# Kernel optimization log

Measured on AMD Instinct MI355X. Metric: run time of the kernel, lower is better.

The kernel has to match this reference:

```python
import jax, jax.numpy as jnp
from jax import lax
import numpy as np

B, CIN, COUT, S = 2, 64, 128, 12
H1, H2 = CIN * 4, COUT * 4          # MBConv hidden dims (expand_ratio=4)
HEADS = 8
MLP_HID = COUT * 4                   # transformer mlp_ratio=4
EPS = 1e-5


def conv1x1(x, w, b=None):
    # 1x1x1 Conv3d == channel matmul. w: [out, in], x: [B,C,H,W,D]
    y = jnp.einsum('oc,bchwd->bohwd', w, x)
    if b is not None:
        y = y + b[None, :, None, None, None]
    return y


def inorm(x, g, b):
    # InstanceNorm3d(affine=True): per-sample, per-channel over spatial dims
    m = x.mean(axis=(2, 3, 4), keepdims=True)
    v = x.var(axis=(2, 3, 4), keepdims=True)
    return (x - m) * jax.lax.rsqrt(v + EPS) * g[None, :, None, None, None] + b[None, :, None, None, None]


def gnorm(x, g, b, groups):
    Bb, C, H, W, D = x.shape
    xr = x.reshape(Bb, groups, C // groups, H, W, D)
    m = xr.mean(axis=(2, 3, 4, 5), keepdims=True)
    v = xr.var(axis=(2, 3, 4, 5), keepdims=True)
    xr = (xr - m) * jax.lax.rsqrt(v + EPS)
    return xr.reshape(Bb, C, H, W, D) * g[None, :, None, None, None] + b[None, :, None, None, None]


def dwconv3(x, w):
    # depthwise 3x3x3, stride 1, pad 1. w: [C,1,3,3,3]
    return lax.conv_general_dilated(
        x, w, window_strides=(1, 1, 1), padding=[(1, 1)] * 3,
        dimension_numbers=('NCDHW', 'OIDHW', 'NCDHW'),
        feature_group_count=x.shape[1])


def mbconv(x, ew, g1, b1, dw, g2, b2, sw1, sb1, sw2, sb2, pw, g3, b3, use_residual):
    res = x
    h = jax.nn.silu(inorm(conv1x1(x, ew), g1, b1))        # expand 1x1
    h = jax.nn.silu(inorm(dwconv3(h, dw), g2, b2))        # depthwise 3x3x3
    s = h.mean(axis=(2, 3, 4), keepdims=True)             # SE: squeeze
    s = jax.nn.silu(conv1x1(s, sw1, sb1))
    s = jax.nn.sigmoid(conv1x1(s, sw2, sb2))
    h = h * s
    h = inorm(conv1x1(h, pw), g3, b3)                     # project
    return res + h if use_residual else h


def mhsa(x, qkv_w, proj_w, proj_b):
    Bb, C, H, W, D = x.shape
    N = H * W * D
    hd = C // HEADS
    qkv = conv1x1(x, qkv_w).reshape(Bb, 3, HEADS, hd, N)
    qkv = jnp.transpose(qkv, (1, 0, 2, 4, 3))             # [3,B,h,N,hd]
    q, k, v = qkv[0], qkv[1], qkv[2]
    attn = jax.nn.softmax(jnp.einsum('bhnd,bhmd->bhnm', q, k) * (hd ** -0.5), axis=-1)
    out = jnp.einsum('bhnm,bhmd->bhnd', attn, v)          # [B,h,N,hd]
    out = jnp.transpose(out, (0, 1, 3, 2)).reshape(Bb, C, H, W, D)
    return conv1x1(out, proj_w, proj_b)


def transformer_block(x, n1g, n1b, qkv, pw, pb, n2g, n2b, mw1, mb1, mw2, mb2):
    x = x + mhsa(gnorm(x, n1g, n1b, min(32, x.shape[1])), qkv, pw, pb)
    h = gnorm(x, n2g, n2b, min(32, x.shape[1]))
    h = conv1x1(jax.nn.gelu(conv1x1(h, mw1, mb1), approximate=False), mw2, mb2)
    return x + h


def shuffle_attn(x, cw1, cw2, gng, gnb, sw):
    b, c, h, w, d = x.shape
    G = 4
    gc = c // (2 * G)  # group_channels
    x6 = x.reshape(b, G, 2 * gc, h, w, d)
    x0 = x6[:, :, :gc].reshape(b * G, gc, h, w, d)
    x1 = x6[:, :, gc:].reshape(b * G, gc, h, w, d)
    # channel branch
    a = x0.mean(axis=(2, 3, 4), keepdims=True)
    a = conv1x1(jax.nn.silu(conv1x1(a, cw1)), cw2)
    x0 = jax.nn.sigmoid(a) * x0
    # spatial branch: GroupNorm(max(1,gc//8)=2 groups) + 1x1 conv
    sgn = gnorm(x1, gng, gnb, max(1, gc // 8))
    x1 = jax.nn.sigmoid(conv1x1(sgn, sw)) * x1
    out = jnp.concatenate([x0.reshape(b, G * gc, h, w, d), x1.reshape(b, G * gc, h, w, d)], axis=1)
    # channel shuffle
    out = out.reshape(b, G, 2 * gc, h, w, d).transpose(0, 2, 1, 3, 4, 5).reshape(b, c, h, w, d)
    return out


def setup_inputs() -> dict:
    key = jax.random.key(0)
    ks = iter(jax.random.split(key, 64))
    w = lambda *shape: jax.random.normal(next(ks), shape, jnp.float32) * 0.05
    p = {}
    p['x'] = jax.random.normal(next(ks), (B, CIN, S, S, S), jnp.float32)
    # mbconv1 (in=64 -> hidden=256 -> out=128), SE reduced = 256//4 = 64
    r1 = H1 // 4
    p['m1_ew'] = w(H1, CIN); p['m1_g1'] = jnp.ones(H1); p['m1_b1'] = jnp.zeros(H1)
    p['m1_dw'] = w(H1, 1, 3, 3, 3); p['m1_g2'] = jnp.ones(H1); p['m1_b2'] = jnp.zeros(H1)
    p['m1_sw1'] = w(r1, H1); p['m1_sb1'] = jnp.zeros(r1)
    p['m1_sw2'] = w(H1, r1); p['m1_sb2'] = jnp.zeros(H1)
    p['m1_pw'] = w(COUT, H1); p['m1_g3'] = jnp.ones(COUT); p['m1_b3'] = jnp.zeros(COUT)
    # mbconv2 (in=128 -> hidden=512 -> out=128, residual), SE reduced = 512//4 = 128
    r2 = H2 // 4
    p['m2_ew'] = w(H2, COUT); p['m2_g1'] = jnp.ones(H2); p['m2_b1'] = jnp.zeros(H2)
    p['m2_dw'] = w(H2, 1, 3, 3, 3); p['m2_g2'] = jnp.ones(H2); p['m2_b2'] = jnp.zeros(H2)
    p['m2_sw1'] = w(r2, H2); p['m2_sb1'] = jnp.zeros(r2)
    p['m2_sw2'] = w(H2, r2); p['m2_sb2'] = jnp.zeros(H2)
    p['m2_pw'] = w(COUT, H2); p['m2_g3'] = jnp.ones(COUT); p['m2_b3'] = jnp.zeros(COUT)
    # transformer
    p['t_n1g'] = jnp.ones(COUT); p['t_n1b'] = jnp.zeros(COUT)
    p['t_qkv'] = w(3 * COUT, COUT)
    p['t_pw'] = w(COUT, COUT); p['t_pb'] = jnp.zeros(COUT)
    p['t_n2g'] = jnp.ones(COUT); p['t_n2b'] = jnp.zeros(COUT)
    p['t_mw1'] = w(MLP_HID, COUT); p['t_mb1'] = jnp.zeros(MLP_HID)
    p['t_mw2'] = w(COUT, MLP_HID); p['t_mb2'] = jnp.zeros(COUT)
    # shuffle attention: group_channels = 128 // 8 = 16, channel_fc reduces to 4
    gc = COUT // 8
    p['s_cw1'] = w(max(1, gc // 4), gc); p['s_cw2'] = w(gc, max(1, gc // 4))
    p['s_gng'] = jnp.ones(gc); p['s_gnb'] = jnp.zeros(gc)
    p['s_sw'] = w(gc, gc)
    return p


def reference(x, m1_ew, m1_g1, m1_b1, m1_dw, m1_g2, m1_b2, m1_sw1, m1_sb1, m1_sw2, m1_sb2, m1_pw, m1_g3, m1_b3, m2_ew, m2_g1, m2_b1, m2_dw, m2_g2, m2_b2, m2_sw1, m2_sb1, m2_sw2, m2_sb2, m2_pw, m2_g3, m2_b3, t_n1g, t_n1b, t_qkv, t_pw, t_pb, t_n2g, t_n2b, t_mw1, t_mb1, t_mw2, t_mb2, s_cw1, s_cw2, s_gng, s_gnb, s_sw):
    x = mbconv(x, m1_ew, m1_g1, m1_b1, m1_dw, m1_g2, m1_b2, m1_sw1, m1_sb1, m1_sw2, m1_sb2, m1_pw, m1_g3, m1_b3, use_residual=False)
    x = mbconv(x, m2_ew, m2_g1, m2_b1, m2_dw, m2_g2, m2_b2, m2_sw1, m2_sb1, m2_sw2, m2_sb2, m2_pw, m2_g3, m2_b3, use_residual=True)
    x = transformer_block(x, t_n1g, t_n1b, t_qkv, t_pw, t_pb, t_n2g, t_n2b, t_mw1, t_mb1, t_mw2, t_mb2)
    x = shuffle_attn(x, s_cw1, s_cw2, s_gng, s_gnb, s_sw)
    return x
```

## Files before the change

kernel.cpp:

```cpp
#include <hip/hip_runtime.h>
#include <cmath>

#define NSP 1728
#define BB  2
#define SS  12

typedef __attribute__((ext_vector_type(8))) short short8;
typedef __attribute__((ext_vector_type(4))) short short4v;
typedef __attribute__((ext_vector_type(4))) float floatx4;

__device__ __forceinline__ short f2bf(float f) {
    unsigned u = __float_as_uint(f);
    u += 0x7fff + ((u >> 16) & 1);
    return (short)(u >> 16);
}
__device__ __forceinline__ unsigned pack2bf(float a, float b) {
    unsigned ua = __float_as_uint(a); ua += 0x7fff + ((ua >> 16) & 1);
    unsigned ub = __float_as_uint(b); ub += 0x7fff + ((ub >> 16) & 1);
    return (ua >> 16) | (ub & 0xffff0000u);
}
__device__ __forceinline__ short8 ld8(const short* p) {
    short4v a = *(const short4v*)p;
    short4v b = *(const short4v*)(p + 4);
    return __builtin_shufflevector(a, b, 0, 1, 2, 3, 4, 5, 6, 7);
}
__device__ __forceinline__ float fexp2(float x) {
    float r;
    asm("v_exp_f32 %0, %1" : "=v"(r) : "v"(x));
    return r;
}

__device__ __forceinline__ void block_reduce2(float& s, float& s2) {
    __shared__ float red[8][2];
    __syncthreads();
    #pragma unroll
    for (int o = 32; o; o >>= 1) {
        s  += __shfl_down(s,  o, 64);
        s2 += __shfl_down(s2, o, 64);
    }
    int lane = threadIdx.x & 63, w = threadIdx.x >> 6;
    if (lane == 0) { red[w][0] = s; red[w][1] = s2; }
    __syncthreads();
    int nw = (blockDim.x + 63) >> 6;
    if (threadIdx.x == 0) {
        float a = 0.f, b = 0.f;
        for (int i = 0; i < nw; i++) { a += red[i][0]; b += red[i][1]; }
        red[0][0] = a; red[0][1] = b;
    }
    __syncthreads();
    s = red[0][0]; s2 = red[0][1];
}

#define WTOT 376832
__global__ __launch_bounds__(256) void prep_kernel(
        const float* __restrict__ s0, const float* __restrict__ s1,
        const float* __restrict__ s2, const float* __restrict__ s3,
        const float* __restrict__ s4, const float* __restrict__ s5,
        const float* __restrict__ s6, const float* __restrict__ s7,
        short* __restrict__ dst, float* __restrict__ stz) {
    if (blockIdx.x < 6) stz[blockIdx.x * 256 + threadIdx.x] = 0.f;
    const int offs[9] = {0, 16384, 49152, 114688, 180224, 229376, 245760, 311296, WTOT};
    const float* srcs[8] = {s0, s1, s2, s3, s4, s5, s6, s7};
    int e = blockIdx.x * 1024 + threadIdx.x * 4;
    #pragma unroll
    for (int k = 0; k < 4; k++) {
        int idx = e + k;
        if (idx >= WTOT) return;
        int seg = 0;
        while (idx >= offs[seg + 1]) seg++;
        dst[idx] = f2bf(srcs[seg][idx - offs[seg]]);
    }
}

template<int CIN, int COUT>
__global__ __launch_bounds__(256) void convm_kernel(
        const float* __restrict__ in, const short* __restrict__ wb,
        const float* __restrict__ biasc,
        const float* __restrict__ se_s,
        const float* __restrict__ sw1, const float* __restrict__ sb1,
        const float* __restrict__ sw2, const float* __restrict__ sb2, int seR,
        const float* __restrict__ fstats, const float* __restrict__ fg,
        const float* __restrict__ fb, int fgs,
        const float* __restrict__ po, const float* __restrict__ pl,
        float* __restrict__ xout,
        const float* resid, float* out, float* stats_out, int act) {
    constexpr int XP = CIN + 8;
    __shared__ float sc[CIN];
    __shared__ float sh[CIN];
    __shared__ float hid[128];
    __shared__ __align__(16) short xa[16 * XP];
    int flat = blockIdx.x;
    int b = flat / 108, mt = flat % 108;
    int n0 = mt * 16;
    int tid = threadIdx.x;

    if (po) {
        if (tid < 128) {
            int hh = tid >> 4, j = tid & 15;
            float l = 0.f;
            #pragma unroll
            for (int js = 0; js < 6; js++)
                l += pl[(size_t)((b * 8 + hh) * 6 + js) * NSP + n0 + j];
            hid[tid] = 1.f / l;
        }
        __syncthreads();
        #pragma unroll
        for (int i = 0; i < CIN / 64; i++) {
            int e = tid + i * 256;
            int ci = e >> 2;
            int jj = (e & 3) * 4;
            int hh = ci >> 4, d = ci & 15;
            float4 acc = {0.f, 0.f, 0.f, 0.f};
            #pragma unroll
            for (int js = 0; js < 6; js++) {
                float4 pv = *(const float4*)(po +
                    ((size_t)((b * 8 + hh) * 6 + js) * 16 + d) * NSP + n0 + jj);
                acc.x += pv.x; acc.y += pv.y; acc.z += pv.z; acc.w += pv.w;
            }
            float4 li = *(const float4*)(hid + hh * 16 + jj);
            xa[(jj + 0) * XP + ci] = f2bf(acc.x * li.x);
            xa[(jj + 1) * XP + ci] = f2bf(acc.y * li.y);
            xa[(jj + 2) * XP + ci] = f2bf(acc.z * li.z);
            xa[(jj + 3) * XP + ci] = f2bf(acc.w * li.w);
        }
        __syncthreads();
    } else {
    if (sw1) {
        for (int c = tid; c < CIN; c += 256) { sc[c] = se_s[b * CIN + c]; sh[c] = 0.f; }
        __syncthreads();
        for (int r = tid; r < seR; r += 256) {
            const float* wr = sw1 + (size_t)r * CIN;
            float h0 = sb1[r], h1 = 0.f, h2 = 0.f, h3 = 0.f;
            for (int c = 0; c < CIN; c += 4) {
                h0 = fmaf(wr[c],     sc[c],     h0);
                h1 = fmaf(wr[c + 1], sc[c + 1], h1);
                h2 = fmaf(wr[c + 2], sc[c + 2], h2);
                h3 = fmaf(wr[c + 3], sc[c + 3], h3);
            }
            float hv = (h0 + h1) + (h2 + h3);
            hid[r] = hv / (1.f + __expf(-hv));
        }
        __syncthreads();
        for (int ci = tid; ci < CIN; ci += 256) {
            const float* wr = sw2 + (size_t)ci * seR;
            float g0 = sb2[ci], g1 = 0.f, g2 = 0.f, g3 = 0.f;
            for (int r = 0; r < seR; r += 4) {
                g0 = fmaf(wr[r],     hid[r],     g0);
                g1 = fmaf(wr[r + 1], hid[r + 1], g1);
                g2 = fmaf(wr[r + 2], hid[r + 2], g2);
                g3 = fmaf(wr[r + 3], hid[r + 3], g3);
            }
            float gv = (g0 + g1) + (g2 + g3);
            sc[ci] = 1.f / (1.f + __expf(-gv));
        }
    } else if (fstats) {
        for (int c = tid; c < CIN; c += 256) {
            int g0 = c / fgs;
            float S = 0.f, S2 = 0.f;
            for (int k = 0; k < fgs; k++) {
                S  += fstats[(b * CIN + g0 * fgs + k) * 2];
                S2 += fstats[(b * CIN + g0 * fgs + k) * 2 + 1];
            }
            float N = fgs * (float)NSP;
            float mean = S / N, var = S2 / N - mean * mean;
            float s = rsqrtf(var + 1e-5f) * fg[c];
            sc[c] = s;
            sh[c] = fb[c] - mean * s;
        }
    } else {
        for (int c = tid; c < CIN; c += 256) { sc[c] = 1.f; sh[c] = 0.f; }
    }
    __syncthreads();

    bool dosw = (xout != nullptr) && (blockIdx.y == 0);
    #pragma unroll
    for (int i = 0; i < CIN / 64; i++) {
        int e = tid + i * 256;
        int ci = e >> 2;
        int jj = (e & 3) * 4;
        size_t gi = ((size_t)b * CIN + ci) * NSP + n0 + jj;
        float4 v4 = *(const float4*)(in + gi);
        float s_ = sc[ci], h_ = sh[ci];
        float v0 = fmaf(v4.x, s_, h_), v1 = fmaf(v4.y, s_, h_);
        float v2 = fmaf(v4.z, s_, h_), v3 = fmaf(v4.w, s_, h_);
        if (dosw) {
            float4 o; o.x = v0; o.y = v1; o.z = v2; o.w = v3;
            *(float4*)(xout + gi) = o;
        }
        xa[(jj + 0) * XP + ci] = f2bf(v0);
        xa[(jj + 1) * XP + ci] = f2bf(v1);
        xa[(jj + 2) * XP + ci] = f2bf(v2);
        xa[(jj + 3) * XP + ci] = f2bf(v3);
    }
    __syncthreads();
    }

    int lane = tid & 63, wv = tid >> 6;
    int col = lane & 15, quad = lane >> 4;
    short8 afr[CIN / 32];
    #pragma unroll
    for (int kc = 0; kc < CIN / 32; kc++)
        afr[kc] = ld8(xa + col * XP + kc * 32 + quad * 8);

    int cobase = blockIdx.y * 64 + wv * 16;
    int co = cobase + col;
    const short* wrow = wb + (size_t)co * CIN;
    floatx4 acc = {0.f, 0.f, 0.f, 0.f};
    #pragma unroll
    for (int kc = 0; kc < CIN / 32; kc++) {
        short8 bw = ld8(wrow + kc * 32 + quad * 8);
        acc = __builtin_amdgcn_mfma_f32_16x16x32_bf16(afr[kc], bw, acc, 0, 0, 0);
    }
    float bv = biasc ? biasc[co] : 0.f;
    float r0 = acc[0] + bv, r1 = acc[1] + bv, r2 = acc[2] + bv, r3 = acc[3] + bv;
    if (act == 2) {
        r0 = 0.5f * r0 * (1.f + erff(r0 * 0.70710678118654752f));
        r1 = 0.5f * r1 * (1.f + erff(r1 * 0.70710678118654752f));
        r2 = 0.5f * r2 * (1.f + erff(r2 * 0.70710678118654752f));
        r3 = 0.5f * r3 * (1.f + erff(r3 * 0.70710678118654752f));
    }
    size_t oi = ((size_t)b * COUT + co) * NSP + n0 + quad * 4;
    if (resid) {
        float4 rv = *(const float4*)(resid + oi);
        r0 += rv.x; r1 += rv.y; r2 += rv.z; r3 += rv.w;
    }
    float4 ov; ov.x = r0; ov.y = r1; ov.z = r2; ov.w = r3;
    *(float4*)(out + oi) = ov;
    if (stats_out) {
        float s  = (r0 + r1) + (r2 + r3);
        float s2 = (r0 * r0 + r1 * r1) + (r2 * r2 + r3 * r3);
        s  += __shfl_xor(s,  16, 64);
        s  += __shfl_xor(s,  32, 64);
        s2 += __shfl_xor(s2, 16, 64);
        s2 += __shfl_xor(s2, 32, 64);
        if (lane < 16) {
            atomicAdd(&stats_out[(b * COUT + cobase + lane) * 2],     s);
            atomicAdd(&stats_out[(b * COUT + cobase + lane) * 2 + 1], s2);
        }
    }
}

__global__ __launch_bounds__(256) void post_kernel(
        const float* __restrict__ p0,
        const float* __restrict__ ng, const float* __restrict__ nb,
        const float* resid, float* out, float* __restrict__ stats_out, int C) {
    int bc = blockIdx.x;
    int c  = bc % C;
    const float* a = p0 + (size_t)bc * NSP;
    float r[7];
    float s = 0.f, s2 = 0.f;
    #pragma unroll
    for (int i = 0; i < 7; i++) {
        int n = threadIdx.x + i * 256;
        if (n < NSP) { r[i] = a[n]; s += r[i]; s2 += r[i] * r[i]; }
        else r[i] = 0.f;
    }
    block_reduce2(s, s2);
    float mean = s / NSP;
    float var = s2 / NSP - mean * mean;
    float rstd = rsqrtf(var + 1e-5f);
    float gc = ng[c], bc2 = nb[c];
    float os = 0.f, os2 = 0.f;
    #pragma unroll
    for (int i = 0; i < 7; i++) {
        int n = threadIdx.x + i * 256;
        if (n < NSP) {
            float v = (r[i] - mean) * rstd * gc + bc2;
            size_t oi = (size_t)bc * NSP + n;
            if (resid) v += resid[oi];
            out[oi] = v;
            os += v; os2 += v * v;
        }
    }
    if (stats_out) {
        block_reduce2(os, os2);
        if (threadIdx.x == 0) {
            stats_out[bc * 2]     = os;
            stats_out[bc * 2 + 1] = os2;
        }
    }
}

__global__ __launch_bounds__(256) void indw_kernel(
        const float* __restrict__ in,
        const float* __restrict__ g1, const float* __restrict__ b1,
        const float* __restrict__ dw,
        const float* __restrict__ g2, const float* __restrict__ b2,
        float* __restrict__ out, float* __restrict__ se_s, int C) {
    int bc = blockIdx.x;
    int c  = bc % C;
    __shared__ float tile[14 * 14 * 14];
    __shared__ float wsh[27];
    const float* ip = in + (size_t)bc * NSP;
    float r[7];
    float s = 0.f, s2 = 0.f;
    for (int i = threadIdx.x; i < 2744; i += 256) tile[i] = 0.f;
    #pragma unroll
    for (int i = 0; i < 7; i++) {
        int n = threadIdx.x + i * 256;
        if (n < NSP) { r[i] = ip[n]; s += r[i]; s2 += r[i] * r[i]; }
        else r[i] = 0.f;
    }
    if (threadIdx.x < 27) wsh[threadIdx.x] = dw[(size_t)c * 27 + threadIdx.x];
    block_reduce2(s, s2);
    float mean = s / NSP, var = s2 / NSP - (s / NSP) * (s / NSP);
    float rstd = rsqrtf(var + 1e-5f);
    float gc = g1[c], bc1 = b1[c];
    #pragma unroll
    for (int i = 0; i < 7; i++) {
        int n = threadIdx.x + i * 256;
        if (n < NSP) {
            int z = n / 144, y = (n / 12) % 12, x = n % 12;
            float v = (r[i] - mean) * rstd * gc + bc1;
            tile[((z + 1) * 14 + y + 1) * 14 + x + 1] = v / (1.f + __expf(-v));
        }
    }
    __syncthreads();
    float d[7];
    #pragma unroll
    for (int i = 0; i < 7; i++) {
        int n = threadIdx.x + i * 256;
        d[i] = 0.f;
        if (n < NSP) {
            int z = n / 144, y = (n / 12) % 12, x = n % 12;
            const float* ctr = tile + ((z + 1) * 14 + y + 1) * 14 + x + 1;
            float acc = 0.f;
            #pragma unroll
            for (int dz = 0; dz < 3; dz++)
                #pragma unroll
                for (int dy = 0; dy < 3; dy++)
                    #pragma unroll
                    for (int dx = 0; dx < 3; dx++)
                        acc = fmaf(wsh[dz * 9 + dy * 3 + dx],
                                   ctr[(dz - 1) * 196 + (dy - 1) * 14 + (dx - 1)], acc);
            d[i] = acc;
        }
    }
    s = 0.f; s2 = 0.f;
    #pragma unroll
    for (int i = 0; i < 7; i++) {
        int n = threadIdx.x + i * 256;
        if (n < NSP) { s += d[i]; s2 += d[i] * d[i]; }
    }
    block_reduce2(s, s2);
    mean = s / NSP; var = s2 / NSP - mean * mean;
    rstd = rsqrtf(var + 1e-5f);
    float gc2 = g2[c], bc2 = b2[c];
    float ssum = 0.f;
    float* op = out + (size_t)bc * NSP;
    #pragma unroll
    for (int i = 0; i < 7; i++) {
        int n = threadIdx.x + i * 256;
        if (n < NSP) {
            float v = (d[i] - mean) * rstd * gc2 + bc2;
            v = v / (1.f + __expf(-v));
            op[n] = v;
            ssum += v;
        }
    }
    float dummy = 0.f;
    block_reduce2(ssum, dummy);
    if (threadIdx.x == 0) se_s[bc] = ssum / NSP;
}

#define AKT 20
#define AVT 296
#define APT 36
#define JCH 288
__global__ __launch_bounds__(256) void attn_split_kernel(const float* __restrict__ qkv,
                                                         float* __restrict__ po,
                                                         float* __restrict__ pl) {
    __shared__ __align__(16) short kt[JCH * AKT];
    __shared__ __align__(16) short vt[16 * AVT];
    __shared__ __align__(16) short pt[4][16 * APT];
    int bh = blockIdx.x;
    int b = bh >> 3, h = bh & 7;
    int js = blockIdx.z;
    int j0 = js * JCH;
    const float* base = qkv + (size_t)b * 384 * NSP;
    const float* qp = base + (size_t)(h * 16) * NSP;
    const float* kp = base + (size_t)(128 + h * 16) * NSP;
    const float* vp = base + (size_t)(256 + h * 16) * NSP;
    for (int t = threadIdx.x; t < 16 * 144; t += 256) {
        int d = t / 144, j = (t - d * 144) * 2;
        float2 kv2 = *(const float2*)(kp + (size_t)d * NSP + j0 + j);
        float2 vv2 = *(const float2*)(vp + (size_t)d * NSP + j0 + j);
        kt[j * AKT + d]       = f2bf(kv2.x);
        kt[(j + 1) * AKT + d] = f2bf(kv2.y);
        *(unsigned*)(vt + d * AVT + j) = pack2bf(vv2.x, vv2.y);
    }
    int wave = threadIdx.x >> 6, lane = threadIdx.x & 63;
    int m = lane & 15, quad = lane >> 4;
    int q0 = (blockIdx.y * 4 + wave) * 16;
    short* ptw = pt[wave];
    short8 qa;
    #pragma unroll
    for (int i = 0; i < 8; i++) qa[i] = 0;
    if (quad < 2) {
        #pragma unroll
        for (int i = 0; i < 8; i++) {
            int d = quad * 8 + i;
            qa[i] = f2bf(qp[(size_t)d * NSP + q0 + m] * 0.36067376022224085f);
        }
    }
    __syncthreads();
    floatx4 o = {0.f, 0.f, 0.f, 0.f};
    float ls = 0.f;
    for (int s = 0; s < 9; s++) {
        int jl = s * 32;
        short8 ak0, ak1;
        #pragma unroll
        for (int i = 0; i < 8; i++) { ak0[i] = 0; ak1[i] = 0; }
        if (quad < 2) {
            ak0 = ld8(kt + (jl + m) * AKT + quad * 8);
            ak1 = ld8(kt + (jl + 16 + m) * AKT + quad * 8);
        }
        floatx4 s0 = {0.f, 0.f, 0.f, 0.f}, s1 = {0.f, 0.f, 0.f, 0.f};
        s0 = __builtin_amdgcn_mfma_f32_16x16x32_bf16(ak0, qa, s0, 0, 0, 0);
        s1 = __builtin_amdgcn_mfma_f32_16x16x32_bf16(ak1, qa, s1, 0, 0, 0);
        float p0r0 = fexp2(s0[0]), p0r1 = fexp2(s0[1]), p0r2 = fexp2(s0[2]), p0r3 = fexp2(s0[3]);
        float p1r0 = fexp2(s1[0]), p1r1 = fexp2(s1[1]), p1r2 = fexp2(s1[2]), p1r3 = fexp2(s1[3]);
        ls += (p0r0 + p0r1) + (p0r2 + p0r3) + (p1r0 + p1r1) + (p1r2 + p1r3);
        uint2 w0, w1;
        w0.x = pack2bf(p0r0, p0r1); w0.y = pack2bf(p0r2, p0r3);
        w1.x = pack2bf(p1r0, p1r1); w1.y = pack2bf(p1r2, p1r3);
        *(uint2*)(ptw + m * APT + quad * 4)      = w0;
        *(uint2*)(ptw + m * APT + 16 + quad * 4) = w1;
        short8 av = ld8(vt + m * AVT + jl + quad * 8);
        short8 pb = ld8(ptw + m * APT + quad * 8);
        o = __builtin_amdgcn_mfma_f32_16x16x32_bf16(av, pb, o, 0, 0, 0);
    }
    ls += __shfl_xor(ls, 16, 64);
    ls += __shfl_xor(ls, 32, 64);
    size_t pbase = ((size_t)(bh * 6 + js) * 16) * NSP;
    #pragma unroll
    for (int r = 0; r < 4; r++)
        po[pbase + (size_t)(quad * 4 + r) * NSP + q0 + m] = o[r];
    if (quad == 0) pl[(size_t)(bh * 6 + js) * NSP + q0 + m] = ls;
}

__global__ void sfinal_kernel(const float* __restrict__ X,
                              const float* __restrict__ st,
                              const float* __restrict__ cw1,
                              const float* __restrict__ cw2,
                              const float* __restrict__ gng,
                              const float* __restrict__ gnb,
                              const float* __restrict__ sw,
                              float* __restrict__ out) {
    int bg = blockIdx.x;
    int b = bg >> 2, g = bg & 3;
    __shared__ float swl[256];
    for (int i = threadIdx.x; i < 256; i += 64) swl[i] = sw[i];
    __syncthreads();
    float pooled[16];
    #pragma unroll
    for (int j = 0; j < 16; j++)
        pooled[j] = st[(b * 128 + g * 32 + j) * 2] * (1.f / NSP);
    float hid[4];
    #pragma unroll
    for (int r = 0; r < 4; r++) {
        float a = 0.f;
        #pragma unroll
        for (int j = 0; j < 16; j++) a = fmaf(cw1[r * 16 + j], pooled[j], a);
        hid[r] = a / (1.f + __expf(-a));
    }
    float gate[16];
    #pragma unroll
    for (int j = 0; j < 16; j++) {
        float a = 0.f;
        #pragma unroll
        for (int r = 0; r < 4; r++) a = fmaf(cw2[j * 4 + r], hid[r], a);
        gate[j] = 1.f / (1.f + __expf(-a));
    }
    float gmean[2], grstd[2];
    #pragma unroll
    for (int t = 0; t < 2; t++) {
        float S = 0.f, S2 = 0.f;
        #pragma unroll
        for (int k = 0; k < 8; k++) {
            int c = g * 32 + 16 + t * 8 + k;
            S  += st[(b * 128 + c) * 2];
            S2 += st[(b * 128 + c) * 2 + 1];
        }
        float N = 8.f * NSP;
        gmean[t] = S / N;
        grstd[t] = rsqrtf(S2 / N - gmean[t] * gmean[t] + 1e-5f);
    }
    int n = blockIdx.y * 64 + threadIdx.x;
    const float* xb = X + (size_t)b * 128 * NSP;
    #pragma unroll
    for (int j = 0; j < 16; j++) {
        float v = xb[(size_t)(g * 32 + j) * NSP + n] * gate[j];
        int k = g * 16 + j;
        int cp = (k % 32) * 4 + (k / 32);
        out[((size_t)b * 128 + cp) * NSP + n] = v;
    }
    float sgn[16];
    #pragma unroll
    for (int j = 0; j < 16; j++) {
        int grp = j >> 3;
        float xv = xb[(size_t)(g * 32 + 16 + j) * NSP + n];
        sgn[j] = (xv - gmean[grp]) * grstd[grp] * gng[j] + gnb[j];
    }
    #pragma unroll
    for (int j = 0; j < 16; j++) {
        float a = 0.f;
        #pragma unroll
        for (int jp = 0; jp < 16; jp++) a = fmaf(swl[j * 16 + jp], sgn[jp], a);
        float v = (1.f / (1.f + __expf(-a))) * xb[(size_t)(g * 32 + 16 + j) * NSP + n];
        int k = 64 + g * 16 + j;
        int cp = (k % 32) * 4 + (k / 32);
        out[((size_t)b * 128 + cp) * NSP + n] = v;
    }
}

extern "C" void kernel_launch(void* const* d_in, const int* in_sizes, int n_in,
                              void* d_out, int out_size, void* d_ws, size_t ws_size,
                              hipStream_t stream) {
    const float* x     = (const float*)d_in[0];
    const float* m1_ew = (const float*)d_in[1];
    const float* m1_g1 = (const float*)d_in[2];
    const float* m1_b1 = (const float*)d_in[3];
    const float* m1_dw = (const float*)d_in[4];
    const float* m1_g2 = (const float*)d_in[5];
    const float* m1_b2 = (const float*)d_in[6];
    const float* m1_sw1= (const float*)d_in[7];
    const float* m1_sb1= (const float*)d_in[8];
    const float* m1_sw2= (const float*)d_in[9];
    const float* m1_sb2= (const float*)d_in[10];
    const float* m1_pw = (const float*)d_in[11];
    const float* m1_g3 = (const float*)d_in[12];
    const float* m1_b3 = (const float*)d_in[13];
    const float* m2_ew = (const float*)d_in[14];
    const float* m2_g1 = (const float*)d_in[15];
    const float* m2_b1 = (const float*)d_in[16];
    const float* m2_dw = (const float*)d_in[17];
    const float* m2_g2 = (const float*)d_in[18];
    const float* m2_b2 = (const float*)d_in[19];
    const float* m2_sw1= (const float*)d_in[20];
    const float* m2_sb1= (const float*)d_in[21];
    const float* m2_sw2= (const float*)d_in[22];
    const float* m2_sb2= (const float*)d_in[23];
    const float* m2_pw = (const float*)d_in[24];
    const float* m2_g3 = (const float*)d_in[25];
    const float* m2_b3 = (const float*)d_in[26];
    const float* t_n1g = (const float*)d_in[27];
    const float* t_n1b = (const float*)d_in[28];
    const float* t_qkv = (const float*)d_in[29];
    const float* t_pw  = (const float*)d_in[30];
    const float* t_pb  = (const float*)d_in[31];
    const float* t_n2g = (const float*)d_in[32];
    const float* t_n2b = (const float*)d_in[33];
    const float* t_mw1 = (const float*)d_in[34];
    const float* t_mb1 = (const float*)d_in[35];
    const float* t_mw2 = (const float*)d_in[36];
    const float* t_mb2 = (const float*)d_in[37];
    const float* s_cw1 = (const float*)d_in[38];
    const float* s_cw2 = (const float*)d_in[39];
    const float* s_gng = (const float*)d_in[40];
    const float* s_gnb = (const float*)d_in[41];
    const float* s_sw  = (const float*)d_in[42];

    float* out = (float*)d_out;

    float* ws = (float*)d_ws;
    float* bufA   = ws;
    float* bufB   = bufA + (size_t)BB * 512 * NSP;
    float* bufX   = bufB + (size_t)BB * 512 * NSP;
    float* bufY   = bufX + (size_t)BB * 128 * NSP;
    float* bufQKV = bufY + (size_t)BB * 128 * NSP;
    float* pl     = bufQKV + (size_t)BB * 384 * NSP;
    float* small  = pl + (size_t)16 * 6 * NSP;
    float* se_s   = small;
    float* st1    = small + 1024;
    float* st3    = small + 1536;
    float* st4    = small + 2048;
    float* st2    = small + 2560;
    short* wbf    = (short*)(small + 8192);
    float* po     = bufA;

    short* W_M1EW = wbf + 0;
    short* W_M1PW = wbf + 16384;
    short* W_M2EW = wbf + 49152;
    short* W_M2PW = wbf + 114688;
    short* W_QKV  = wbf + 180224;
    short* W_TPW  = wbf + 229376;
    short* W_MW1  = wbf + 245760;
    short* W_MW2  = wbf + 311296;

    dim3 blk(256);

    prep_kernel<<<(WTOT + 1023) / 1024, blk, 0, stream>>>(
        m1_ew, m1_pw, m2_ew, m2_pw, t_qkv, t_pw, t_mw1, t_mw2, wbf, st1);

    convm_kernel<64, 256><<<dim3(BB * 108, 4), blk, 0, stream>>>(
        x, W_M1EW, nullptr,
        nullptr, nullptr, nullptr, nullptr, nullptr, 0,
        nullptr, nullptr, nullptr, 0,
        nullptr, nullptr, nullptr,
        nullptr, bufA, nullptr, 0);
    indw_kernel<<<BB * 256, blk, 0, stream>>>(bufA, m1_g1, m1_b1, m1_dw, m1_g2, m1_b2, bufB, se_s, 256);
    convm_kernel<256, 128><<<dim3(BB * 108, 2), blk, 0, stream>>>(
        bufB, W_M1PW, nullptr,
        se_s, m1_sw1, m1_sb1, m1_sw2, m1_sb2, 64,
        nullptr, nullptr, nullptr, 0,
        nullptr, nullptr, nullptr,
        nullptr, bufY, st1, 0);

    convm_kernel<128, 512><<<dim3(BB * 108, 8), blk, 0, stream>>>(
        bufY, W_M2EW, nullptr,
        nullptr, nullptr, nullptr, nullptr, nullptr, 0,
        st1, m1_g3, m1_b3, 1,
        nullptr, nullptr, bufX,
        nullptr, bufA, nullptr, 0);
    indw_kernel<<<BB * 512, blk, 0, stream>>>(bufA, m2_g1, m2_b1, m2_dw, m2_g2, m2_b2, bufB, se_s, 512);
    convm_kernel<512, 128><<<dim3(BB * 108, 2), blk, 0, stream>>>(
        bufB, W_M2PW, nullptr,
        se_s, m2_sw1, m2_sb1, m2_sw2, m2_sb2, 128,
        nullptr, nullptr, nullptr, 0,
        nullptr, nullptr, nullptr,
        nullptr, bufY, nullptr, 0);
    post_kernel<<<BB * 128, blk, 0, stream>>>(bufY, m2_g3, m2_b3, bufX, bufX, st2, 128);

    convm_kernel<128, 384><<<dim3(BB * 108, 6), blk, 0, stream>>>(
        bufX, W_QKV, nullptr,
        nullptr, nullptr, nullptr, nullptr, nullptr, 0,
        st2, t_n1g, t_n1b, 4,
        nullptr, nullptr, nullptr,
        nullptr, bufQKV, nullptr, 0);
    attn_split_kernel<<<dim3(16, 27, 6), blk, 0, stream>>>(bufQKV, po, pl);
    convm_kernel<128, 128><<<dim3(BB * 108, 2), blk, 0, stream>>>(
        nullptr, W_TPW, t_pb,
        nullptr, nullptr, nullptr, nullptr, nullptr, 0,
        nullptr, nullptr, nullptr, 0,
        po, pl, nullptr,
        bufX, bufX, st3, 0);
    convm_kernel<128, 512><<<dim3(BB * 108, 8), blk, 0, stream>>>(
        bufX, W_MW1, t_mb1,
        nullptr, nullptr, nullptr, nullptr, nullptr, 0,
        st3, t_n2g, t_n2b, 4,
        nullptr, nullptr, nullptr,
        nullptr, bufA, nullptr, 2);
    convm_kernel<512, 128><<<dim3(BB * 108, 2), blk, 0, stream>>>(
        bufA, W_MW2, t_mb2,
        nullptr, nullptr, nullptr, nullptr, nullptr, 0,
        nullptr, nullptr, nullptr, 0,
        nullptr, nullptr, nullptr,
        bufX, bufX, st4, 0);

    sfinal_kernel<<<dim3(BB * 4, 27), dim3(64), 0, stream>>>(
        bufX, st4, s_cw1, s_cw2, s_gng, s_gnb, s_sw, out);
}
```

Baseline: 342.5 us.

## Fuse post-norm residual into QKV conv via algebraic stats; transpose SE weights

Removes the separate post_kernel that applied the second MBConv's instance norm plus residual. The projection conv now accumulates five per-channel moments (sum, sum of squares, cross term with the residual, residual sum, residual sum of squares) by atomics. The QKV conv then reconstructs the group-norm statistics of the normalized-plus-residual tensor algebraically and applies both normalizations while loading its input. SE weights are also pre-transposed in the prep kernel so per-thread reads become coalesced. This saves a full read and write pass over the activation, at the cost of extra atomics, an extra residual read in two convs, and possible precision loss from computing variance as E[x^2]-mean^2.

After: 333.8 us. -2.5%, faster.

```diff
diff --git a/kernel.cpp b/kernel.cpp
--- a/kernel.cpp
+++ b/kernel.cpp
@@ -57,15 +57,40 @@
         const float* __restrict__ s2, const float* __restrict__ s3,
         const float* __restrict__ s4, const float* __restrict__ s5,
         const float* __restrict__ s6, const float* __restrict__ s7,
-        short* __restrict__ dst, float* __restrict__ stz) {
-    if (blockIdx.x < 6) stz[blockIdx.x * 256 + threadIdx.x] = 0.f;
+        short* __restrict__ dst, float* __restrict__ stz,
+        const float* __restrict__ w1a, const float* __restrict__ w2a,
+        const float* __restrict__ w1b, const float* __restrict__ w2b,
+        float* __restrict__ tsw) {
+    if (blockIdx.x < 11) stz[blockIdx.x * 256 + threadIdx.x] = 0.f;
+    if (blockIdx.x >= 368) {
+        int e = (blockIdx.x - 368) * 1024 + threadIdx.x * 4;
+        #pragma unroll
+        for (int k = 0; k < 4; k++) {
+            int idx = e + k;
+            float v;
+            if (idx < 16384) {
+                int c = idx >> 6, r = idx & 63;
+                v = w1a[r * 256 + c];
+            } else if (idx < 32768) {
+                int l = idx - 16384; int r = l >> 8, ci = l & 255;
+                v = w2a[ci * 64 + r];
+            } else if (idx < 98304) {
+                int l = idx - 32768; int c = l >> 7, r = l & 127;
+                v = w1b[r * 512 + c];
+            } else {
+                int l = idx - 98304; int r = l >> 9, ci = l & 511;
+                v = w2b[ci * 128 + r];
+            }
+            tsw[idx] = v;
+        }
+        return;
+    }
     const int offs[9] = {0, 16384, 49152, 114688, 180224, 229376, 245760, 311296, WTOT};
     const float* srcs[8] = {s0, s1, s2, s3, s4, s5, s6, s7};
     int e = blockIdx.x * 1024 + threadIdx.x * 4;
     #pragma unroll
     for (int k = 0; k < 4; k++) {
         int idx = e + k;
-        if (idx >= WTOT) return;
         int seg = 0;
         while (idx >= offs[seg + 1]) seg++;
         dst[idx] = f2bf(srcs[seg][idx - offs[seg]]);
@@ -81,12 +106,17 @@
         const float* __restrict__ sw2, const float* __restrict__ sb2, int seR,
         const float* __restrict__ fstats, const float* __restrict__ fg,
         const float* __restrict__ fb, int fgs,
+        const float* __restrict__ ing, const float* __restrict__ inb,
+        const float* __restrict__ inres,
         const float* __restrict__ po, const float* __restrict__ pl,
         float* __restrict__ xout,
-        const float* resid, float* out, float* stats_out, int act) {
+        const float* resid, float* out, float* stats_out,
+        const float* __restrict__ statres, int act) {
     constexpr int XP = CIN + 8;
     __shared__ float sc[CIN];
     __shared__ float sh[CIN];
+    __shared__ float sa[CIN];
+    __shared__ float sbl[CIN];
     __shared__ float hid[128];
     __shared__ __align__(16) short xa[16 * XP];
     int flat = blockIdx.x;
@@ -129,29 +159,54 @@
         for (int c = tid; c < CIN; c += 256) { sc[c] = se_s[b * CIN + c]; sh[c] = 0.f; }
         __syncthreads();
         for (int r = tid; r < seR; r += 256) {
-            const float* wr = sw1 + (size_t)r * CIN;
             float h0 = sb1[r], h1 = 0.f, h2 = 0.f, h3 = 0.f;
             for (int c = 0; c < CIN; c += 4) {
-                h0 = fmaf(wr[c],     sc[c],     h0);
-                h1 = fmaf(wr[c + 1], sc[c + 1], h1);
-                h2 = fmaf(wr[c + 2], sc[c + 2], h2);
-                h3 = fmaf(wr[c + 3], sc[c + 3], h3);
+                h0 = fmaf(sw1[(c + 0) * seR + r], sc[c],     h0);
+                h1 = fmaf(sw1[(c + 1) * seR + r], sc[c + 1], h1);
+                h2 = fmaf(sw1[(c + 2) * seR + r], sc[c + 2], h2);
+                h3 = fmaf(sw1[(c + 3) * seR + r], sc[c + 3], h3);
             }
             float hv = (h0 + h1) + (h2 + h3);
             hid[r] = hv / (1.f + __expf(-hv));
         }
         __syncthreads();
         for (int ci = tid; ci < CIN; ci += 256) {
-            const float* wr = sw2 + (size_t)ci * seR;
             float g0 = sb2[ci], g1 = 0.f, g2 = 0.f, g3 = 0.f;
             for (int r = 0; r < seR; r += 4) {
-                g0 = fmaf(wr[r],     hid[r],     g0);
-                g1 = fmaf(wr[r + 1], hid[r + 1], g1);
-                g2 = fmaf(wr[r + 2], hid[r + 2], g2);
-                g3 = fmaf(wr[r + 3], hid[r + 3], g3);
+                g0 = fmaf(sw2[(r + 0) * CIN + ci], hid[r],     g0);
+                g1 = fmaf(sw2[(r + 1) * CIN + ci], hid[r + 1], g1);
+                g2 = fmaf(sw2[(r + 2) * CIN + ci], hid[r + 2], g2);
+                g3 = fmaf(sw2[(r + 3) * CIN + ci], hid[r + 3], g3);
             }
             float gv = (g0 + g1) + (g2 + g3);
             sc[ci] = 1.f / (1.f + __expf(-gv));
+        }
+    } else if (ing) {
+        for (int c = tid; c < CIN; c += 256) {
+            const float* S = fstats + (size_t)(b * CIN + c) * 5;
+            float A = S[0], Bq = S[1], Cq = S[2], Dq = S[3], Eq = S[4];
+            const float N = (float)NSP;
+            float mean = A / N, var = Bq / N - mean * mean;
+            float a_ = ing[c] * rsqrtf(var + 1e-5f);
+            float b_ = inb[c] - mean * a_;
+            sa[c] = a_; sbl[c] = b_;
+            sc[c] = a_ * A + b_ * N + Dq;
+            sh[c] = a_ * a_ * Bq + 2.f * a_ * b_ * A + b_ * b_ * N
+                  + 2.f * a_ * Cq + 2.f * b_ * Dq + Eq;
+        }
+        __syncthreads();
+        float gS = 0.f, gS2 = 0.f;
+        if (tid < CIN) {
+            int g0 = (tid / fgs) * fgs;
+            for (int k = 0; k < fgs; k++) { gS += sc[g0 + k]; gS2 += sh[g0 + k]; }
+        }
+        __syncthreads();
+        if (tid < CIN) {
+            float Ng = fgs * (float)NSP;
+            float gm = gS / Ng, gv = gS2 / Ng - gm * gm;
+            float s_ = rsqrtf(gv + 1e-5f) * fg[tid];
+            sc[tid] = s_;
+            sh[tid] = fb[tid] - gm * s_;
         }
     } else if (fstats) {
         for (int c = tid; c < CIN; c += 256) {
@@ -180,12 +235,29 @@
         int jj = (e & 3) * 4;
         size_t gi = ((size_t)b * CIN + ci) * NSP + n0 + jj;
         float4 v4 = *(const float4*)(in + gi);
-        float s_ = sc[ci], h_ = sh[ci];
-        float v0 = fmaf(v4.x, s_, h_), v1 = fmaf(v4.y, s_, h_);
-        float v2 = fmaf(v4.z, s_, h_), v3 = fmaf(v4.w, s_, h_);
-        if (dosw) {
-            float4 o; o.x = v0; o.y = v1; o.z = v2; o.w = v3;
-            *(float4*)(xout + gi) = o;
+        float v0, v1, v2, v3;
+        if (ing) {
+            float4 rr = *(const float4*)(inres + gi);
+            float a_ = sa[ci], b_ = sbl[ci];
+            float x0 = fmaf(v4.x, a_, b_) + rr.x;
+            float x1 = fmaf(v4.y, a_, b_) + rr.y;
+            float x2 = fmaf(v4.z, a_, b_) + rr.z;
+            float x3 = fmaf(v4.w, a_, b_) + rr.w;
+            if (dosw) {
+                float4 o; o.x = x0; o.y = x1; o.z = x2; o.w = x3;
+                *(float4*)(xout + gi) = o;
+            }
+            float s_ = sc[ci], h_ = sh[ci];
+            v0 = fmaf(x0, s_, h_); v1 = fmaf(x1, s_, h_);
+            v2 = fmaf(x2, s_, h_); v3 = fmaf(x3, s_, h_);
+        } else {
+            float s_ = sc[ci], h_ = sh[ci];
+            v0 = fmaf(v4.x, s_, h_); v1 = fmaf(v4.y, s_, h_);
+            v2 = fmaf(v4.z, s_, h_); v3 = fmaf(v4.w, s_, h_);
+            if (dosw) {
+                float4 o; o.x = v0; o.y = v1; o.z = v2; o.w = v3;
+                *(float4*)(xout + gi) = o;
+            }
         }
         xa[(jj + 0) * XP + ci] = f2bf(v0);
         xa[(jj + 1) * XP + ci] = f2bf(v1);
@@ -227,56 +299,37 @@
     float4 ov; ov.x = r0; ov.y = r1; ov.z = r2; ov.w = r3;
     *(float4*)(out + oi) = ov;
     if (stats_out) {
-        float s  = (r0 + r1) + (r2 + r3);
-        float s2 = (r0 * r0 + r1 * r1) + (r2 * r2 + r3 * r3);
-        s  += __shfl_xor(s,  16, 64);
-        s  += __shfl_xor(s,  32, 64);
-        s2 += __shfl_xor(s2, 16, 64);
-        s2 += __shfl_xor(s2, 32, 64);
-        if (lane < 16) {
-            atomicAdd(&stats_out[(b * COUT + cobase + lane) * 2],     s);
-            atomicAdd(&stats_out[(b * COUT + cobase + lane) * 2 + 1], s2);
-        }
-    }
-}
-
-__global__ __launch_bounds__(256) void post_kernel(
-        const float* __restrict__ p0,
-        const float* __restrict__ ng, const float* __restrict__ nb,
-        const float* resid, float* out, float* __restrict__ stats_out, int C) {
-    int bc = blockIdx.x;
-    int c  = bc % C;
-    const float* a = p0 + (size_t)bc * NSP;
-    float r[7];
-    float s = 0.f, s2 = 0.f;
-    #pragma unroll
-    for (int i = 0; i < 7; i++) {
-        int n = threadIdx.x + i * 256;
-        if (n < NSP) { r[i] = a[n]; s += r[i]; s2 += r[i] * r[i]; }
-        else r[i] = 0.f;
-    }
-    block_reduce2(s, s2);
-    float mean = s / NSP;
-    float var = s2 / NSP - mean * mean;
-    float rstd = rsqrtf(var + 1e-5f);
-    float gc = ng[c], bc2 = nb[c];
-    float os = 0.f, os2 = 0.f;
-    #pragma unroll
-    for (int i = 0; i < 7; i++) {
-        int n = threadIdx.x + i * 256;
-        if (n < NSP) {
-            float v = (r[i] - mean) * rstd * gc + bc2;
-            size_t oi = (size_t)bc * NSP + n;
-            if (resid) v += resid[oi];
-            out[oi] = v;
-            os += v; os2 += v * v;
-        }
-    }
-    if (stats_out) {
-        block_reduce2(os, os2);
-        if (threadIdx.x == 0) {
-            stats_out[bc * 2]     = os;
-            stats_out[bc * 2 + 1] = os2;
+        if (statres) {
+            float4 rv = *(const float4*)(statres + oi);
+            float s   = (r0 + r1) + (r2 + r3);
+            float s2  = (r0 * r0 + r1 * r1) + (r2 * r2 + r3 * r3);
+            float sx  = (r0 * rv.x + r1 * rv.y) + (r2 * rv.z + r3 * rv.w);
+            float sr  = (rv.x + rv.y) + (rv.z + rv.w);
+            float sr2 = (rv.x * rv.x + rv.y * rv.y) + (rv.z * rv.z + rv.w * rv.w);
+            s   += __shfl_xor(s,   16, 64); s   += __shfl_xor(s,   32, 64);
+            s2  += __shfl_xor(s2,  16, 64); s2  += __shfl_xor(s2,  32, 64);
+            sx  += __shfl_xor(sx,  16, 64); sx  += __shfl_xor(sx,  32, 64);
+            sr  += __shfl_xor(sr,  16, 64); sr  += __shfl_xor(sr,  32, 64);
+            sr2 += __shfl_xor(sr2, 16, 64); sr2 += __shfl_xor(sr2, 32, 64);
+            if (lane < 16) {
+                float* sp = stats_out + (size_t)(b * COUT + cobase + lane) * 5;
+                atomicAdd(sp + 0, s);
+                atomicAdd(sp + 1, s2);
+                atomicAdd(sp + 2, sx);
+                atomicAdd(sp + 3, sr);
+                atomicAdd(sp + 4, sr2);
+            }
+        } else {
+            float s  = (r0 + r1) + (r2 + r3);
+            float s2 = (r0 * r0 + r1 * r1) + (r2 * r2 + r3 * r3);
+            s  += __shfl_xor(s,  16, 64);
+            s  += __shfl_xor(s,  32, 64);
+            s2 += __shfl_xor(s2, 16, 64);
+            s2 += __shfl_xor(s2, 32, 64);
+            if (lane < 16) {
+                atomicAdd(&stats_out[(b * COUT + cobase + lane) * 2],     s);
+                atomicAdd(&stats_out[(b * COUT + cobase + lane) * 2 + 1], s2);
+            }
         }
     }
 }
@@ -577,6 +630,12 @@
     float* st4    = small + 2048;
     float* st2    = small + 2560;
     short* wbf    = (short*)(small + 8192);
+    float* tsw    = small + 196608;
+    float* T_M1SW1 = tsw;
+    float* T_M1SW2 = tsw + 16384;
+    float* T_M2SW1 = tsw + 32768;
+    float* T_M2SW2 = tsw + 98304;
+    float* bufX2  = tsw + 163840;
     float* po     = bufA;
 
     short* W_M1EW = wbf + 0;
@@ -590,64 +649,72 @@
 
     dim3 blk(256);
 
-    prep_kernel<<<(WTOT + 1023) / 1024, blk, 0, stream>>>(
-        m1_ew, m1_pw, m2_ew, m2_pw, t_qkv, t_pw, t_mw1, t_mw2, wbf, st1);
+    prep_kernel<<<528, blk, 0, stream>>>(
+        m1_ew, m1_pw, m2_ew, m2_pw, t_qkv, t_pw, t_mw1, t_mw2, wbf, st1,
+        m1_sw1, m1_sw2, m2_sw1, m2_sw2, tsw);
 
     convm_kernel<64, 256><<<dim3(BB * 108, 4), blk, 0, stream>>>(
         x, W_M1EW, nullptr,
         nullptr, nullptr, nullptr, nullptr, nullptr, 0,
         nullptr, nullptr, nullptr, 0,
         nullptr, nullptr, nullptr,
-        nullptr, bufA, nullptr, 0);
+        nullptr, nullptr, nullptr,
+        nullptr, bufA, nullptr, nullptr, 0);
     indw_kernel<<<BB * 256, blk, 0, stream>>>(bufA, m1_g1, m1_b1, m1_dw, m1_g2, m1_b2, bufB, se_s, 256);
     convm_kernel<256, 128><<<dim3(BB * 108, 2), blk, 0, stream>>>(
         bufB, W_M1PW, nullptr,
-        se_s, m1_sw1, m1_sb1, m1_sw2, m1_sb2, 64,
+        se_s, T_M1SW1, m1_sb1, T_M1SW2, m1_sb2, 64,
         nullptr, nullptr, nullptr, 0,
         nullptr, nullptr, nullptr,
-        nullptr, bufY, st1, 0);
+        nullptr, nullptr, nullptr,
+        nullptr, bufY, st1, nullptr, 0);
 
     convm_kernel<128, 512><<<dim3(BB * 108, 8), blk, 0, stream>>>(
         bufY, W_M2EW, nullptr,
         nullptr, nullptr, nullptr, nullptr, nullptr, 0,
         st1, m1_g3, m1_b3, 1,
+        nullptr, nullptr, nullptr,
         nullptr, nullptr, bufX,
-        nullptr, bufA, nullptr, 0);
+        nullptr, bufA, nullptr, nullptr, 0);
     indw_kernel<<<BB * 512, blk, 0, stream>>>(bufA, m2_g1, m2_b1, m2_dw, m2_g2, m2_b2, bufB, se_s, 512);
     convm_kernel<512, 128><<<dim3(BB * 108, 2), blk, 0, stream>>>(
         bufB, W_M2PW, nullptr,
-        se_s, m2_sw1, m2_sb1, m2_sw2, m2_sb2, 128,
+        se_s, T_M2SW1, m2_sb1, T_M2SW2, m2_sb2, 128,
         nullptr, nullptr, nullptr, 0,
         nullptr, nullptr, nullptr,
-        nullptr, bufY, nullptr, 0);
-    post_kernel<<<BB * 128, blk, 0, stream>>>(bufY, m2_g3, m2_b3, bufX, bufX, st2, 128);
+        nullptr, nullptr, nullptr,
+        nullptr, bufY, st2, bufX, 0);
 
     convm_kernel<128, 384><<<dim3(BB * 108, 6), blk, 0, stream>>>(
-        bufX, W_QKV, nullptr,
+        bufY, W_QKV, nullptr,
         nullptr, nullptr, nullptr, nullptr, nullptr, 0,
         st2, t_n1g, t_n1b, 4,
-        nullptr, nullptr, nullptr,
-        nullptr, bufQKV, nullptr, 0);
+        m2_g3, m2_b3, bufX,
+        nullptr, nullptr, bufX2,
+        nullptr, bufQKV, nullptr, nullptr, 0);
     attn_split_kernel<<<dim3(16, 27, 6), blk, 0, stream>>>(bufQKV, po, pl);
     convm_kernel<128, 128><<<dim3(BB * 108, 2), blk, 0, stream>>>(
         nullptr, W_TPW, t_pb,
         nullptr, nullptr, nullptr, nullptr, nullptr, 0,
         nullptr, nullptr, nullptr, 0,
+        nullptr, nullptr, nullptr,
         po, pl, nullptr,
-        bufX, bufX, st3, 0);
+        bufX2, bufX2, st3, nullptr, 0);
     convm_kernel<128, 512><<<dim3(BB * 108, 8), blk, 0, stream>>>(
-        bufX, W_MW1, t_mb1,
+        bufX2, W_MW1, t_mb1,
         nullptr, nullptr, nullptr, nullptr, nullptr, 0,
         st3, t_n2g, t_n2b, 4,
         nullptr, nullptr, nullptr,
-        nullptr, bufA, nullptr, 2);
+        nullptr, nullptr, nullptr,
+        nullptr, bufA, nullptr, nullptr, 2);
     convm_kernel<512, 128><<<dim3(BB * 108, 2), blk, 0, stream>>>(
         bufA, W_MW2, t_mb2,
         nullptr, nullptr, nullptr, nullptr, nullptr, 0,
         nullptr, nullptr, nullptr, 0,
         nullptr, nullptr, nullptr,
-        bufX, bufX, st4, 0);
+        nullptr, nullptr, nullptr,
+        bufX2, bufX2, st4, nullptr, 0);
 
     sfinal_kernel<<<dim3(BB * 4, 27), dim3(64), 0, stream>>>(
-        bufX, st4, s_cw1, s_cw2, s_gng, s_gnb, s_sw, out);
-}
+        bufX2, st4, s_cw1, s_cw2, s_gng, s_gnb, s_sw, out);
+}
```
